# Kernel tuning notes

Hardware: AMD Instinct MI355X
Metric: run time of the kernel (lower is better)

The kernel has to match this reference:

```python
import jax, jax.numpy as jnp
import numpy as np

HEAD_DIM = 64  # config['head_dim']
# dropout_prob=0.1 is a no-op in eval mode; reference computes deterministic attention.

def setup_inputs() -> dict:
    key = jax.random.key(0)
    kq, kk, kv = jax.random.split(key, 3)
    shape = (2, 12, 2048, HEAD_DIM)  # [batch, heads, seq, head_dim]
    Q = jax.random.normal(kq, shape, dtype=jnp.float32)
    K = jax.random.normal(kk, shape, dtype=jnp.float32)
    V = jax.random.normal(kv, shape, dtype=jnp.float32)
    return {"Q": Q, "K": K, "V": V}

def reference(Q, K, V):
    # dot = Q @ K^T / sqrt(head_dim); attn = softmax(dot); X = attn @ V
    scale = 1.0 / np.float32(np.sqrt(HEAD_DIM))
    dot = jnp.einsum('bhqd,bhkd->bhqk', Q, K) * scale  # [B,H,S,S]
    attn = jax.nn.softmax(dot, axis=-1)
    X = jnp.einsum('bhqk,bhkd->bhqd', attn, V)
    return X
```

## Files before the change

kernel.cpp:

```cpp
#include <hip/hip_runtime.h>
#include <hip/hip_bf16.h>

typedef __attribute__((ext_vector_type(8))) short bf16x8;
typedef __attribute__((ext_vector_type(4))) float f32x4;
typedef __attribute__((ext_vector_type(4))) unsigned short u16x4;
typedef __attribute__((ext_vector_type(2))) unsigned int u32x2;
typedef __attribute__((ext_vector_type(4))) unsigned int u32x4;
typedef __attribute__((ext_vector_type(4))) _Float16 f16x4;
typedef __attribute__((ext_vector_type(8))) _Float16 f16x8;
typedef __attribute__((ext_vector_type(2))) __fp16 h16x2;
typedef __attribute__((ext_vector_type(4))) __fp16 h16x4;

#define SEQ 2048
#define HD 64
#define BH 24

__device__ __forceinline__ unsigned bfpack(float a, float b) {
  union { float f; unsigned u; } ua, ub; ua.f = a; ub.f = b;
  return __builtin_amdgcn_perm(ub.u + 0x8000u, ua.u + 0x8000u, 0x07060302u);
}
__device__ __forceinline__ unsigned short f2bf(float f) {
  union { float f; unsigned u; } v; v.f = f;
  unsigned r = v.u + 0x7fffu + ((v.u >> 16) & 1u);
  return (unsigned short)(r >> 16);
}

__global__ __launch_bounds__(256) void prep_kv(const float* __restrict__ K,
                                               const float* __restrict__ V,
                                               unsigned* __restrict__ Kb,
                                               _Float16* __restrict__ Vt) {
  __shared__ _Float16 t[64 * 68];
  const int bh = blockIdx.y;
  const int k0 = blockIdx.x * 64;
  const int tid = threadIdx.x;

  const float4* ks = (const float4*)(K + ((size_t)bh * SEQ + k0) * HD);
  unsigned* kd = Kb + ((size_t)bh * SEQ + k0) * (HD / 2);
#pragma unroll
  for (int i = 0; i < 4; ++i) {
    int f = tid + i * 256;
    float4 v = ks[f];
    u32x2 o;
    o.x = bfpack(v.x, v.y);
    o.y = bfpack(v.z, v.w);
    *(u32x2*)&kd[f * 2] = o;
  }

  const float4* vs = (const float4*)(V + ((size_t)bh * SEQ + k0) * HD);
#pragma unroll
  for (int i = 0; i < 4; ++i) {
    int f = tid + i * 256;
    int k = f >> 4, cg = f & 15;
    float4 v = vs[k * 16 + cg];
    int dg = cg * 4;
    t[(dg + 0) * 68 + k] = (_Float16)v.x;
    t[(dg + 1) * 68 + k] = (_Float16)v.y;
    t[(dg + 2) * 68 + k] = (_Float16)v.z;
    t[(dg + 3) * 68 + k] = (_Float16)v.w;
  }
  __syncthreads();
  int d = tid >> 2, kg = (tid & 3) * 16;
  _Float16* g = Vt + ((size_t)(bh * 64 + d)) * SEQ + k0 + kg;
#pragma unroll
  for (int r = 0; r < 4; ++r) {
    f16x4 x = *(f16x4*)&t[d * 68 + kg + r * 4];
    *(f16x4*)&g[r * 4] = x;
  }
}

__global__ __launch_bounds__(512, 5) void attn_main(const float* __restrict__ Q,
                                                    const unsigned short* __restrict__ Kb,
                                                    const _Float16* __restrict__ Vt,
                                                    float* __restrict__ O) {
  __shared__ unsigned short kv[3][8192];

  const int tid  = threadIdx.x;
  const int lane = tid & 63;
  const int w    = tid >> 6;
  const int kq   = w & 3;
  const int qh   = w >> 2;
  const int quad = lane >> 4;
  const int n    = lane & 15;

  const int bh = blockIdx.x;
  const int q0 = blockIdx.y * 64;

  const float qscale = 0.125f * 1.44269504088896f;

  bf16x8 qf[2][2];
#pragma unroll
  for (int u = 0; u < 2; ++u) {
    const float* qb = Q + ((size_t)bh * SEQ + q0 + qh * 32 + u * 16 + n) * HD;
#pragma unroll
    for (int h = 0; h < 2; ++h) {
      float4 a = *(const float4*)(qb + h * 32 + quad * 8);
      float4 b = *(const float4*)(qb + h * 32 + quad * 8 + 4);
      u32x4 pk;
      pk.x = bfpack(a.x * qscale, a.y * qscale);
      pk.y = bfpack(a.z * qscale, a.w * qscale);
      pk.z = bfpack(b.x * qscale, b.y * qscale);
      pk.w = bfpack(b.z * qscale, b.w * qscale);
      qf[u][h] = __builtin_bit_cast(bf16x8, pk);
    }
  }

  const unsigned short* Kbase = Kb + (size_t)bh * SEQ * HD;
  const unsigned short* Vbase = (const unsigned short*)(Vt + (size_t)bh * HD * SEQ);
  const int r_ = tid >> 3, p_ = tid & 7, G_ = p_ ^ (r_ & 7);
  const unsigned short* ksrc = Kbase + r_ * HD + G_ * 8;
  const unsigned short* vsrc = Vbase + (size_t)r_ * SEQ + G_ * 8;
  const int soff = tid * 8;

#define DMA_TO(buf_, it_)                                                                 \
  {                                                                                       \
    unsigned short* db_ = &kv[buf_][0];                                                   \
    __builtin_amdgcn_global_load_lds(                                                     \
        (const __attribute__((address_space(1))) void*)(ksrc + (size_t)(it_) * 4096),     \
        (__attribute__((address_space(3))) void*)(db_ + soff), 16, 0, 0);                 \
    __builtin_amdgcn_global_load_lds(                                                     \
        (const __attribute__((address_space(1))) void*)(vsrc + (size_t)(it_) * 64),       \
        (__attribute__((address_space(3))) void*)(db_ + 4096 + soff), 16, 0, 0);          \
    asm volatile("" ::: "memory");                                                        \
  }

  f32x4 o[4][2];
#pragma unroll
  for (int dt = 0; dt < 4; ++dt)
#pragma unroll
    for (int u = 0; u < 2; ++u) o[dt][u] = (f32x4){0.f, 0.f, 0.f, 0.f};
  float lsum[2] = {0.f, 0.f};

  int ro[2];
#pragma unroll
  for (int h = 0; h < 2; ++h)
    ro[h] = (kq * 16 + n) * 64 + (((h * 4 + quad) ^ (n & 7)) * 8);
  int vo[4];
#pragma unroll
  for (int dt = 0; dt < 4; ++dt)
    vo[dt] = (dt * 16 + n) * 64 + (((kq * 2 + (quad >> 1)) ^ (n & 7)) * 8) + (quad & 1) * 4;

#define COMPUTE(buf_)                                                                     \
  {                                                                                       \
    const unsigned short* kb = &kv[buf_][0];                                              \
    const unsigned short* vb = kb + 4096;                                                 \
    f32x4 s[2] = {{0,0,0,0},{0,0,0,0}};                                                   \
    _Pragma("unroll")                                                                     \
    for (int h = 0; h < 2; ++h) {                                                         \
      bf16x8 a = *(const bf16x8*)&kb[ro[h]];                                              \
      _Pragma("unroll")                                                                   \
      for (int u = 0; u < 2; ++u)                                                         \
        s[u] = __builtin_amdgcn_mfma_f32_16x16x32_bf16(a, qf[u][h], s[u], 0, 0, 0);       \
    }                                                                                     \
    f16x4 pf[2];                                                                          \
    _Pragma("unroll")                                                                     \
    for (int u = 0; u < 2; ++u) {                                                         \
      float e0 = __builtin_amdgcn_exp2f(s[u][0]);                                         \
      float e1 = __builtin_amdgcn_exp2f(s[u][1]);                                         \
      float e2 = __builtin_amdgcn_exp2f(s[u][2]);                                         \
      float e3 = __builtin_amdgcn_exp2f(s[u][3]);                                         \
      lsum[u] += (e0 + e1) + (e2 + e3);                                                   \
      h16x2 a_ = __builtin_amdgcn_cvt_pkrtz(e0, e1);                                      \
      h16x2 b_ = __builtin_amdgcn_cvt_pkrtz(e2, e3);                                      \
      h16x4 ab_ = __builtin_shufflevector(a_, b_, 0, 1, 2, 3);                            \
      pf[u] = __builtin_bit_cast(f16x4, ab_);                                             \
    }                                                                                     \
    _Pragma("unroll")                                                                     \
    for (int dt = 0; dt < 4; ++dt) {                                                      \
      f16x4 vf = *(const f16x4*)((const _Float16*)vb + vo[dt]);                           \
      _Pragma("unroll")                                                                   \
      for (int u = 0; u < 2; ++u)                                                         \
        o[dt][u] = __builtin_amdgcn_mfma_f32_16x16x16f16(vf, pf[u], o[dt][u], 0, 0, 0);   \
    }                                                                                     \
  }

  DMA_TO(0, 0);
  DMA_TO(1, 1);

  int bc = 0;
  int bd = 2;
  for (int it = 0; it < 31; ++it) {
    asm volatile("s_waitcnt vmcnt(2)\n\ts_barrier" ::: "memory");
    if (it < 30) DMA_TO(bd, it + 2);
    COMPUTE(bc);
    bc = (bc == 2) ? 0 : bc + 1;
    bd = (bd == 2) ? 0 : bd + 1;
  }
  asm volatile("s_waitcnt vmcnt(0)\n\ts_barrier" ::: "memory");
  COMPUTE(bc);

#undef DMA_TO
#undef COMPUTE

#pragma unroll
  for (int u = 0; u < 2; ++u) {
    lsum[u] += __shfl_xor(lsum[u], 16);
    lsum[u] += __shfl_xor(lsum[u], 32);
  }

  float* red = (float*)&kv[0][0];
  float* lred = red + 4 * 2048;

  __syncthreads();
  if (kq >= 2) {
    int slot = qh * 2 + (kq - 2);
#pragma unroll
    for (int dt = 0; dt < 4; ++dt)
#pragma unroll
      for (int u = 0; u < 2; ++u)
        *(f32x4*)&red[slot * 2048 + (dt * 2 + u) * 256 + lane * 4] = o[dt][u];
#pragma unroll
    for (int u = 0; u < 2; ++u) lred[slot * 128 + u * 64 + lane] = lsum[u];
  }
  __syncthreads();
  if (kq < 2) {
    int slot = qh * 2 + kq;
#pragma unroll
    for (int dt = 0; dt < 4; ++dt)
#pragma unroll
      for (int u = 0; u < 2; ++u)
        o[dt][u] += *(f32x4*)&red[slot * 2048 + (dt * 2 + u) * 256 + lane * 4];
#pragma unroll
    for (int u = 0; u < 2; ++u) lsum[u] += lred[slot * 128 + u * 64 + lane];
  }
  __syncthreads();
  if (kq == 1) {
#pragma unroll
    for (int dt = 0; dt < 4; ++dt)
#pragma unroll
      for (int u = 0; u < 2; ++u)
        *(f32x4*)&red[qh * 2048 + (dt * 2 + u) * 256 + lane * 4] = o[dt][u];
#pragma unroll
    for (int u = 0; u < 2; ++u) lred[qh * 128 + u * 64 + lane] = lsum[u];
  }
  __syncthreads();
  if (kq == 0) {
#pragma unroll
    for (int u = 0; u < 2; ++u) {
      float ltot = lsum[u];
#pragma unroll
      for (int dt = 0; dt < 4; ++dt)
        o[dt][u] += *(f32x4*)&red[qh * 2048 + (dt * 2 + u) * 256 + lane * 4];
      ltot += lred[qh * 128 + u * 64 + lane];
      float inv = 1.0f / ltot;
      float* og = O + ((size_t)bh * SEQ + q0 + qh * 32 + u * 16 + n) * HD + quad * 4;
#pragma unroll
      for (int dt = 0; dt < 4; ++dt) {
        f32x4 r = o[dt][u];
        r.x *= inv; r.y *= inv; r.z *= inv; r.w *= inv;
        *(f32x4*)(og + dt * 16) = r;
      }
    }
  }
}

#define F_QT 128
#define F_KT 64
#define F_LD 72

__global__ __launch_bounds__(512) void attn_fwd(const float* __restrict__ Q,
                                                const float* __restrict__ K,
                                                const float* __restrict__ V,
                                                float* __restrict__ O) {
  __shared__ unsigned short sm[(F_QT + F_KT + HD + 8 * 16) * F_LD];
  unsigned short* Qs = sm;
  unsigned short* Ks = Qs + F_QT * F_LD;
  unsigned short* Vt = Ks + F_KT * F_LD;
  unsigned short* Ps = Vt + HD * F_LD;

  const int tid = threadIdx.x, lane = tid & 63, wv = tid >> 6;
  const int quad = lane >> 4, n = lane & 15;
  const int bh = blockIdx.y, q0 = blockIdx.x * F_QT;
  const float* Qg = Q + ((size_t)bh * SEQ + q0) * HD;
  const float* Kg = K + (size_t)bh * SEQ * HD;
  const float* Vg = V + (size_t)bh * SEQ * HD;
  float* Og = O + ((size_t)bh * SEQ + q0) * HD;
  const float qscale = 0.125f * 1.44269504088896f;

#pragma unroll
  for (int i = 0; i < 4; ++i) {
    int f = tid + i * 512;
    int row = f >> 4, cg = f & 15;
    float4 qv = ((const float4*)Qg)[row * 16 + cg];
    u16x4 h;
    h.x = f2bf(qv.x * qscale); h.y = f2bf(qv.y * qscale);
    h.z = f2bf(qv.z * qscale); h.w = f2bf(qv.w * qscale);
    *(u16x4*)&Qs[row * F_LD + cg * 4] = h;
  }
  __syncthreads();
  bf16x8 qf0 = *(const bf16x8*)&Qs[(wv * 16 + n) * F_LD + quad * 8];
  bf16x8 qf1 = *(const bf16x8*)&Qs[(wv * 16 + n) * F_LD + 32 + quad * 8];
  f32x4 o[4] = {{0,0,0,0},{0,0,0,0},{0,0,0,0},{0,0,0,0}};
  float mrow[4] = {-1e30f,-1e30f,-1e30f,-1e30f};
  float lrow[4] = {0.f,0.f,0.f,0.f};
  unsigned short* Pw = Ps + wv * 16 * F_LD;

  for (int it = 0; it < SEQ / F_KT; ++it) {
    __syncthreads();
    const float* Ktg = Kg + (size_t)it * F_KT * HD;
    const float* Vtg = Vg + (size_t)it * F_KT * HD;
#pragma unroll
    for (int i = 0; i < 2; ++i) {
      int f = tid + i * 512;
      int row = f >> 4, cg = f & 15;
      float4 kvv = ((const float4*)Ktg)[row * 16 + cg];
      u16x4 hk;
      hk.x = f2bf(kvv.x); hk.y = f2bf(kvv.y); hk.z = f2bf(kvv.z); hk.w = f2bf(kvv.w);
      *(u16x4*)&Ks[row * F_LD + cg * 4] = hk;
      float4 vv = ((const float4*)Vtg)[row * 16 + cg];
      Vt[(cg * 4 + 0) * F_LD + row] = f2bf(vv.x);
      Vt[(cg * 4 + 1) * F_LD + row] = f2bf(vv.y);
      Vt[(cg * 4 + 2) * F_LD + row] = f2bf(vv.z);
      Vt[(cg * 4 + 3) * F_LD + row] = f2bf(vv.w);
    }
    __syncthreads();
    f32x4 s[4];
#pragma unroll
    for (int t = 0; t < 4; ++t) {
      bf16x8 b0 = *(const bf16x8*)&Ks[(t * 16 + n) * F_LD + quad * 8];
      bf16x8 b1 = *(const bf16x8*)&Ks[(t * 16 + n) * F_LD + 32 + quad * 8];
      f32x4 c = {0,0,0,0};
      c = __builtin_amdgcn_mfma_f32_16x16x32_bf16(qf0, b0, c, 0, 0, 0);
      c = __builtin_amdgcn_mfma_f32_16x16x32_bf16(qf1, b1, c, 0, 0, 0);
      s[t] = c;
    }
    float mnew[4], alpha[4], rsum[4];
#pragma unroll
    for (int r = 0; r < 4; ++r) {
      float ml = fmaxf(fmaxf(s[0][r], s[1][r]), fmaxf(s[2][r], s[3][r]));
      ml = fmaxf(ml, __shfl_xor(ml, 1));
      ml = fmaxf(ml, __shfl_xor(ml, 2));
      ml = fmaxf(ml, __shfl_xor(ml, 4));
      ml = fmaxf(ml, __shfl_xor(ml, 8));
      mnew[r] = fmaxf(mrow[r], ml);
      alpha[r] = __builtin_amdgcn_exp2f(mrow[r] - mnew[r]);
      mrow[r] = mnew[r];
      rsum[r] = 0.f;
    }
#pragma unroll
    for (int t = 0; t < 4; ++t)
#pragma unroll
      for (int r = 0; r < 4; ++r) {
        float p = __builtin_amdgcn_exp2f(s[t][r] - mnew[r]);
        rsum[r] += p;
        Pw[(quad * 4 + r) * F_LD + t * 16 + n] = f2bf(p);
      }
#pragma unroll
    for (int r = 0; r < 4; ++r) {
      float rs = rsum[r];
      rs += __shfl_xor(rs, 1); rs += __shfl_xor(rs, 2);
      rs += __shfl_xor(rs, 4); rs += __shfl_xor(rs, 8);
      lrow[r] = lrow[r] * alpha[r] + rs;
      o[0][r] *= alpha[r]; o[1][r] *= alpha[r];
      o[2][r] *= alpha[r]; o[3][r] *= alpha[r];
    }
    asm volatile("s_waitcnt lgkmcnt(0)" ::: "memory");
    bf16x8 p0 = *(const bf16x8*)&Pw[n * F_LD + quad * 8];
    bf16x8 p1 = *(const bf16x8*)&Pw[n * F_LD + 32 + quad * 8];
#pragma unroll
    for (int t = 0; t < 4; ++t) {
      bf16x8 v0 = *(const bf16x8*)&Vt[(t * 16 + n) * F_LD + quad * 8];
      bf16x8 v1 = *(const bf16x8*)&Vt[(t * 16 + n) * F_LD + 32 + quad * 8];
      o[t] = __builtin_amdgcn_mfma_f32_16x16x32_bf16(p0, v0, o[t], 0, 0, 0);
      o[t] = __builtin_amdgcn_mfma_f32_16x16x32_bf16(p1, v1, o[t], 0, 0, 0);
    }
  }
  float inv[4];
#pragma unroll
  for (int r = 0; r < 4; ++r) inv[r] = 1.0f / lrow[r];
#pragma unroll
  for (int t = 0; t < 4; ++t)
#pragma unroll
    for (int r = 0; r < 4; ++r)
      Og[(wv * 16 + quad * 4 + r) * HD + t * 16 + n] = o[t][r] * inv[r];
}

extern "C" void kernel_launch(void* const* d_in, const int* in_sizes, int n_in,
                              void* d_out, int out_size, void* d_ws, size_t ws_size,
                              hipStream_t stream) {
  const float* Q = (const float*)d_in[0];
  const float* K = (const float*)d_in[1];
  const float* V = (const float*)d_in[2];
  float* O = (float*)d_out;

  const size_t mat = (size_t)BH * SEQ * HD;
  const size_t need = 2 * mat * sizeof(unsigned short);

  if (ws_size >= need) {
    unsigned short* Kb = (unsigned short*)d_ws;
    _Float16* Vt = (_Float16*)(Kb + mat);
    prep_kv<<<dim3(SEQ / 64, BH), 256, 0, stream>>>(K, V, (unsigned*)Kb, Vt);
    attn_main<<<dim3(BH, SEQ / 64), 512, 0, stream>>>(Q, Kb, Vt, O);
  } else {
    attn_fwd<<<dim3(SEQ / F_QT, BH), 512, 0, stream>>>(Q, K, V, O);
  }
}
```

Before: 119.9 us.

## Double query tile per block to reuse K/V tiles across more rows

Each block now handles 128 query rows instead of 64, so each wave carries four 16-row query fragments and reuses each loaded K/V fragment across twice as many MFMAs. This halves the grid and the total K/V traffic through LDS per query row, and amortizes the DMA and barrier cost. The cross-wave reduction is restructured to fit the larger accumulators in the same shared buffer by reducing in two halves over head-dim, which adds more barriers. The launch-bounds occupancy hint is dropped, so register use rises and occupancy likely falls.

```diff
diff --git a/kernel.cpp b/kernel.cpp
--- a/kernel.cpp
+++ b/kernel.cpp
@@ -68,10 +68,10 @@
   }
 }
 
-__global__ __launch_bounds__(512, 5) void attn_main(const float* __restrict__ Q,
-                                                    const unsigned short* __restrict__ Kb,
-                                                    const _Float16* __restrict__ Vt,
-                                                    float* __restrict__ O) {
+__global__ __launch_bounds__(512) void attn_main(const float* __restrict__ Q,
+                                                 const unsigned short* __restrict__ Kb,
+                                                 const _Float16* __restrict__ Vt,
+                                                 float* __restrict__ O) {
   __shared__ unsigned short kv[3][8192];
 
   const int tid  = threadIdx.x;
@@ -83,14 +83,14 @@
   const int n    = lane & 15;
 
   const int bh = blockIdx.x;
-  const int q0 = blockIdx.y * 64;
+  const int q0 = blockIdx.y * 128;
 
   const float qscale = 0.125f * 1.44269504088896f;
 
-  bf16x8 qf[2][2];
-#pragma unroll
-  for (int u = 0; u < 2; ++u) {
-    const float* qb = Q + ((size_t)bh * SEQ + q0 + qh * 32 + u * 16 + n) * HD;
+  bf16x8 qf[4][2];
+#pragma unroll
+  for (int u = 0; u < 4; ++u) {
+    const float* qb = Q + ((size_t)bh * SEQ + q0 + qh * 64 + u * 16 + n) * HD;
 #pragma unroll
     for (int h = 0; h < 2; ++h) {
       float4 a = *(const float4*)(qb + h * 32 + quad * 8);
@@ -123,12 +123,12 @@
     asm volatile("" ::: "memory");                                                        \
   }
 
-  f32x4 o[4][2];
+  f32x4 o[4][4];
 #pragma unroll
   for (int dt = 0; dt < 4; ++dt)
 #pragma unroll
-    for (int u = 0; u < 2; ++u) o[dt][u] = (f32x4){0.f, 0.f, 0.f, 0.f};
-  float lsum[2] = {0.f, 0.f};
+    for (int u = 0; u < 4; ++u) o[dt][u] = (f32x4){0.f, 0.f, 0.f, 0.f};
+  float lsum[4] = {0.f, 0.f, 0.f, 0.f};
 
   int ro[2];
 #pragma unroll
@@ -143,17 +143,17 @@
   {                                                                                       \
     const unsigned short* kb = &kv[buf_][0];                                              \
     const unsigned short* vb = kb + 4096;                                                 \
-    f32x4 s[2] = {{0,0,0,0},{0,0,0,0}};                                                   \
+    bf16x8 a0 = *(const bf16x8*)&kb[ro[0]];                                               \
+    bf16x8 a1 = *(const bf16x8*)&kb[ro[1]];                                               \
+    f32x4 s[4] = {{0,0,0,0},{0,0,0,0},{0,0,0,0},{0,0,0,0}};                               \
     _Pragma("unroll")                                                                     \
-    for (int h = 0; h < 2; ++h) {                                                         \
-      bf16x8 a = *(const bf16x8*)&kb[ro[h]];                                              \
-      _Pragma("unroll")                                                                   \
-      for (int u = 0; u < 2; ++u)                                                         \
-        s[u] = __builtin_amdgcn_mfma_f32_16x16x32_bf16(a, qf[u][h], s[u], 0, 0, 0);       \
+    for (int u = 0; u < 4; ++u) {                                                         \
+      s[u] = __builtin_amdgcn_mfma_f32_16x16x32_bf16(a0, qf[u][0], s[u], 0, 0, 0);        \
+      s[u] = __builtin_amdgcn_mfma_f32_16x16x32_bf16(a1, qf[u][1], s[u], 0, 0, 0);        \
     }                                                                                     \
-    f16x4 pf[2];                                                                          \
+    f16x4 pf[4];                                                                          \
     _Pragma("unroll")                                                                     \
-    for (int u = 0; u < 2; ++u) {                                                         \
+    for (int u = 0; u < 4; ++u) {                                                         \
       float e0 = __builtin_amdgcn_exp2f(s[u][0]);                                         \
       float e1 = __builtin_amdgcn_exp2f(s[u][1]);                                         \
       float e2 = __builtin_amdgcn_exp2f(s[u][2]);                                         \
@@ -168,7 +168,7 @@
     for (int dt = 0; dt < 4; ++dt) {                                                      \
       f16x4 vf = *(const f16x4*)((const _Float16*)vb + vo[dt]);                           \
       _Pragma("unroll")                                                                   \
-      for (int u = 0; u < 2; ++u)                                                         \
+      for (int u = 0; u < 4; ++u)                                                         \
         o[dt][u] = __builtin_amdgcn_mfma_f32_16x16x16f16(vf, pf[u], o[dt][u], 0, 0, 0);   \
     }                                                                                     \
   }
@@ -192,7 +192,7 @@
 #undef COMPUTE
 
 #pragma unroll
-  for (int u = 0; u < 2; ++u) {
+  for (int u = 0; u < 4; ++u) {
     lsum[u] += __shfl_xor(lsum[u], 16);
     lsum[u] += __shfl_xor(lsum[u], 32);
   }
@@ -201,48 +201,71 @@
   float* lred = red + 4 * 2048;
 
   __syncthreads();
-  if (kq >= 2) {
-    int slot = qh * 2 + (kq - 2);
-#pragma unroll
-    for (int dt = 0; dt < 4; ++dt)
-#pragma unroll
-      for (int u = 0; u < 2; ++u)
-        *(f32x4*)&red[slot * 2048 + (dt * 2 + u) * 256 + lane * 4] = o[dt][u];
-#pragma unroll
-    for (int u = 0; u < 2; ++u) lred[slot * 128 + u * 64 + lane] = lsum[u];
-  }
-  __syncthreads();
-  if (kq < 2) {
-    int slot = qh * 2 + kq;
-#pragma unroll
-    for (int dt = 0; dt < 4; ++dt)
-#pragma unroll
-      for (int u = 0; u < 2; ++u)
-        o[dt][u] += *(f32x4*)&red[slot * 2048 + (dt * 2 + u) * 256 + lane * 4];
-#pragma unroll
-    for (int u = 0; u < 2; ++u) lsum[u] += lred[slot * 128 + u * 64 + lane];
-  }
-  __syncthreads();
-  if (kq == 1) {
-#pragma unroll
-    for (int dt = 0; dt < 4; ++dt)
-#pragma unroll
-      for (int u = 0; u < 2; ++u)
-        *(f32x4*)&red[qh * 2048 + (dt * 2 + u) * 256 + lane * 4] = o[dt][u];
-#pragma unroll
-    for (int u = 0; u < 2; ++u) lred[qh * 128 + u * 64 + lane] = lsum[u];
+  if (kq & 1) {
+    int slot = qh * 2 + (kq >> 1);
+#pragma unroll
+    for (int u = 0; u < 4; ++u) lred[slot * 256 + u * 64 + lane] = lsum[u];
+  }
+  __syncthreads();
+  if (!(kq & 1)) {
+    int slot = qh * 2 + (kq >> 1);
+#pragma unroll
+    for (int u = 0; u < 4; ++u) lsum[u] += lred[slot * 256 + u * 64 + lane];
+  }
+  __syncthreads();
+  if (kq == 2) {
+#pragma unroll
+    for (int u = 0; u < 4; ++u) lred[qh * 256 + u * 64 + lane] = lsum[u];
   }
   __syncthreads();
   if (kq == 0) {
 #pragma unroll
-    for (int u = 0; u < 2; ++u) {
-      float ltot = lsum[u];
-#pragma unroll
-      for (int dt = 0; dt < 4; ++dt)
-        o[dt][u] += *(f32x4*)&red[qh * 2048 + (dt * 2 + u) * 256 + lane * 4];
-      ltot += lred[qh * 128 + u * 64 + lane];
-      float inv = 1.0f / ltot;
-      float* og = O + ((size_t)bh * SEQ + q0 + qh * 32 + u * 16 + n) * HD + quad * 4;
+    for (int u = 0; u < 4; ++u) lsum[u] += lred[qh * 256 + u * 64 + lane];
+  }
+
+#pragma unroll
+  for (int dp = 0; dp < 2; ++dp) {
+    __syncthreads();
+    if (kq & 1) {
+      int slot = qh * 2 + (kq >> 1);
+#pragma unroll
+      for (int d2 = 0; d2 < 2; ++d2)
+#pragma unroll
+        for (int u = 0; u < 4; ++u)
+          *(f32x4*)&red[slot * 2048 + (d2 * 4 + u) * 256 + lane * 4] = o[dp * 2 + d2][u];
+    }
+    __syncthreads();
+    if (!(kq & 1)) {
+      int slot = qh * 2 + (kq >> 1);
+#pragma unroll
+      for (int d2 = 0; d2 < 2; ++d2)
+#pragma unroll
+        for (int u = 0; u < 4; ++u)
+          o[dp * 2 + d2][u] += *(f32x4*)&red[slot * 2048 + (d2 * 4 + u) * 256 + lane * 4];
+    }
+    __syncthreads();
+    if (kq == 2) {
+#pragma unroll
+      for (int d2 = 0; d2 < 2; ++d2)
+#pragma unroll
+        for (int u = 0; u < 4; ++u)
+          *(f32x4*)&red[qh * 2048 + (d2 * 4 + u) * 256 + lane * 4] = o[dp * 2 + d2][u];
+    }
+    __syncthreads();
+    if (kq == 0) {
+#pragma unroll
+      for (int d2 = 0; d2 < 2; ++d2)
+#pragma unroll
+        for (int u = 0; u < 4; ++u)
+          o[dp * 2 + d2][u] += *(f32x4*)&red[qh * 2048 + (d2 * 4 + u) * 256 + lane * 4];
+    }
+  }
+
+  if (kq == 0) {
+#pragma unroll
+    for (int u = 0; u < 4; ++u) {
+      float inv = 1.0f / lsum[u];
+      float* og = O + ((size_t)bh * SEQ + q0 + qh * 64 + u * 16 + n) * HD + quad * 4;
 #pragma unroll
       for (int dt = 0; dt < 4; ++dt) {
         f32x4 r = o[dt][u];
@@ -389,7 +412,7 @@
     unsigned short* Kb = (unsigned short*)d_ws;
     _Float16* Vt = (_Float16*)(Kb + mat);
     prep_kv<<<dim3(SEQ / 64, BH), 256, 0, stream>>>(K, V, (unsigned*)Kb, Vt);
-    attn_main<<<dim3(BH, SEQ / 64), 512, 0, stream>>>(Q, Kb, Vt, O);
+    attn_main<<<dim3(BH, SEQ / 128), 512, 0, stream>>>(Q, Kb, Vt, O);
   } else {
     attn_fwd<<<dim3(SEQ / F_QT, BH), 512, 0, stream>>>(Q, K, V, O);
   }
```

Result: slower. 134.7 us (+12.3%).
